# Optimization experiments

Measured on AMD Instinct MI355X. Metric: run time of the kernel, lower is better.

Reference implementation:

```python
import jax, jax.numpy as jnp
import numpy as np
import math

B, S, H = 2, 2048, 2048
NH, NKV, HD = 16, 8, 128          # heads, kv heads, head_dim
GROUPS = NH // NKV                 # 2
FF = 5632
EPS = 1e-6
SCALE = 0.02


def setup_inputs() -> dict:
    key = jax.random.key(0)
    ks = jax.random.split(key, 12)
    def w(k, shape):
        return jax.random.normal(k, shape, dtype=jnp.float32) * SCALE
    # additive causal mask: 0 on/below diagonal, -inf above
    causal = jnp.where(jnp.tril(jnp.ones((S, S), dtype=bool)), 0.0, -jnp.inf)
    attention_mask = causal[None, None].astype(jnp.float32)  # [1,1,S,S]
    return {
        "hidden_states": jax.random.normal(ks[0], (B, S, H), dtype=jnp.float32),
        "attention_mask": attention_mask,
        "q_w": w(ks[1], (NH * HD, H)),      # nn.Linear convention [out, in]
        "k_w": w(ks[2], (NKV * HD, H)),
        "v_w": w(ks[3], (NKV * HD, H)),
        "o_w": w(ks[4], (H, NH * HD)),
        "gate_w": w(ks[5], (FF, H)),
        "up_w": w(ks[6], (FF, H)),
        "down_w": w(ks[7], (H, FF)),
        "ln1_w": jnp.ones((H,), dtype=jnp.float32),
        "ln2_w": jnp.ones((H,), dtype=jnp.float32),
    }


def rmsnorm(x, w):
    var = jnp.mean(jnp.square(x), axis=-1, keepdims=True)
    return x * jax.lax.rsqrt(var + EPS) * w


def attention(x, mask, q_w, k_w, v_w, o_w):
    b, s, _ = x.shape
    q = (x @ q_w.T).reshape(b, s, NH, HD).transpose(0, 2, 1, 3)    # [b,nh,s,hd]
    k = (x @ k_w.T).reshape(b, s, NKV, HD).transpose(0, 2, 1, 3)   # [b,nkv,s,hd]
    v = (x @ v_w.T).reshape(b, s, NKV, HD).transpose(0, 2, 1, 3)
    # GQA: repeat_interleave kv heads to match query heads
    k = jnp.repeat(k, GROUPS, axis=1)
    v = jnp.repeat(v, GROUPS, axis=1)
    scores = jnp.einsum("bhqd,bhkd->bhqk", q, k) / math.sqrt(HD) + mask
    probs = jax.nn.softmax(scores.astype(jnp.float32), axis=-1).astype(q.dtype)
    out = jnp.einsum("bhqk,bhkd->bhqd", probs, v)
    out = out.transpose(0, 2, 1, 3).reshape(b, s, NH * HD)
    return out @ o_w.T


def mlp(x, gate_w, up_w, down_w):
    return (jax.nn.silu(x @ gate_w.T) * (x @ up_w.T)) @ down_w.T


def reference(hidden_states, attention_mask, q_w, k_w, v_w, o_w,
              gate_w, up_w, down_w, ln1_w, ln2_w):
    # pre-norm transformer layer with residuals
    h = hidden_states + attention(rmsnorm(hidden_states, ln1_w), attention_mask,
                                  q_w, k_w, v_w, o_w)
    out = h + mlp(rmsnorm(h, ln2_w), gate_w, up_w, down_w)
    return out
```

## Files before the change

kernel.cpp:

```cpp
#include <hip/hip_runtime.h>
#include <stdint.h>

typedef __bf16 bf16_t;
typedef __bf16 bf16x8 __attribute__((ext_vector_type(8)));
typedef __bf16 bf16x4 __attribute__((ext_vector_type(4)));
typedef float  f32x4  __attribute__((ext_vector_type(4)));

#define MFMA16(a, b, c) __builtin_amdgcn_mfma_f32_16x16x32_bf16((a), (b), (c), 0, 0, 0)

__device__ __forceinline__ void load_lds16(const bf16_t* g, bf16_t* l)
{
    __builtin_amdgcn_global_load_lds(
        (const __attribute__((address_space(1))) uint32_t*)(uintptr_t)g,
        (__attribute__((address_space(3))) uint32_t*)(uint32_t)(uintptr_t)l,
        16, 0, 0);
}

__global__ __launch_bounds__(256)
void wconv(const float* __restrict__ X, bf16_t* __restrict__ Y, int n)
{
    int i = (blockIdx.x * 256 + threadIdx.x) * 8;
    if (i >= n) return;
    f32x4 a = *(const f32x4*)(X + i);
    f32x4 b = *(const f32x4*)(X + i + 4);
    bf16x8 y;
#pragma unroll
    for (int e = 0; e < 4; ++e) { y[e] = (bf16_t)a[e]; y[e + 4] = (bf16_t)b[e]; }
    *(bf16x8*)(Y + i) = y;
}

__global__ __launch_bounds__(256)
void rmsnorm_f32(const float* __restrict__ X, const float* __restrict__ Wt,
                 bf16_t* __restrict__ Y)
{
    __shared__ float red[4];
    const int tid = threadIdx.x;
    const size_t row = blockIdx.x;
    const float* x = X + row * 2048;

    f32x4 x0 = *(const f32x4*)(x + tid * 8);
    f32x4 x1 = *(const f32x4*)(x + tid * 8 + 4);
    float ss = 0.f;
#pragma unroll
    for (int e = 0; e < 4; ++e) ss += x0[e] * x0[e] + x1[e] * x1[e];
#pragma unroll
    for (int off = 32; off; off >>= 1) ss += __shfl_xor(ss, off, 64);
    if ((tid & 63) == 0) red[tid >> 6] = ss;
    __syncthreads();
    float tot = red[0] + red[1] + red[2] + red[3];
    float scale = rsqrtf(tot * (1.f / 2048.f) + 1e-6f);

    f32x4 w0 = *(const f32x4*)(Wt + tid * 8);
    f32x4 w1 = *(const f32x4*)(Wt + tid * 8 + 4);
    bf16x8 yv;
#pragma unroll
    for (int e = 0; e < 4; ++e) {
        yv[e]     = (bf16_t)(x0[e] * scale * w0[e]);
        yv[e + 4] = (bf16_t)(x1[e] * scale * w1[e]);
    }
    *(bf16x8*)(Y + row * 2048 + tid * 8) = yv;
}

__global__ __launch_bounds__(256)
void rmsnorm_bf16(const bf16_t* __restrict__ X, const float* __restrict__ Wt,
                  bf16_t* __restrict__ Y)
{
    __shared__ float red[4];
    const int tid = threadIdx.x;
    const size_t row = blockIdx.x;

    bf16x8 xv = *(const bf16x8*)(X + row * 2048 + tid * 8);
    float xf[8];
    float ss = 0.f;
#pragma unroll
    for (int e = 0; e < 8; ++e) { xf[e] = (float)xv[e]; ss += xf[e] * xf[e]; }
#pragma unroll
    for (int off = 32; off; off >>= 1) ss += __shfl_xor(ss, off, 64);
    if ((tid & 63) == 0) red[tid >> 6] = ss;
    __syncthreads();
    float tot = red[0] + red[1] + red[2] + red[3];
    float scale = rsqrtf(tot * (1.f / 2048.f) + 1e-6f);

    f32x4 w0 = *(const f32x4*)(Wt + tid * 8);
    f32x4 w1 = *(const f32x4*)(Wt + tid * 8 + 4);
    bf16x8 yv;
#pragma unroll
    for (int e = 0; e < 4; ++e) {
        yv[e]     = (bf16_t)(xf[e] * scale * w0[e]);
        yv[e + 4] = (bf16_t)(xf[e + 4] * scale * w1[e]);
    }
    *(bf16x8*)(Y + row * 2048 + tid * 8) = yv;
}

__global__ __launch_bounds__(256, 2)
void gemm_bb(const bf16_t* __restrict__ A, const bf16_t* __restrict__ W,
             const float* __restrict__ Rf, const bf16_t* __restrict__ Rb,
             bf16_t* __restrict__ Cb, float* __restrict__ Cf,
             int M, int N, int K, int mode)
{
    __shared__ bf16_t As[128 * 64];
    __shared__ bf16_t Ws[128 * 64];

    const int tid  = threadIdx.x;
    const int lane = tid & 63, wave = tid >> 6;
    const int quad = lane >> 4, l16 = lane & 15;
    const int m0 = blockIdx.y * 128, n0 = blockIdx.x * 128;
    const int wm = (wave >> 1) * 64, wn = (wave & 1) * 64;

    const bf16_t* Ab = A + (size_t)(m0 + (tid >> 3)) * K + ((tid & 7) << 3);
    const bf16_t* Wb = W + (size_t)(n0 + (tid >> 3)) * K + ((tid & 7) << 3);

    f32x4 acc[4][4] = {};

    for (int k0 = 0; k0 < K; k0 += 64) {
        __syncthreads();
#pragma unroll
        for (int i = 0; i < 4; ++i) {
            load_lds16(Ab + (size_t)(i * 32) * K + k0, As + (i * 256 + tid) * 8);
            load_lds16(Wb + (size_t)(i * 32) * K + k0, Ws + (i * 256 + tid) * 8);
        }
        __syncthreads();

#pragma unroll
        for (int ks = 0; ks < 64; ks += 32) {
            bf16x8 af[4], bfr[4];
#pragma unroll
            for (int i = 0; i < 4; ++i)
                af[i] = *(const bf16x8*)(As + (wm + i * 16 + l16) * 64 + ks + quad * 8);
#pragma unroll
            for (int j = 0; j < 4; ++j)
                bfr[j] = *(const bf16x8*)(Ws + (wn + j * 16 + l16) * 64 + ks + quad * 8);
#pragma unroll
            for (int i = 0; i < 4; ++i)
#pragma unroll
                for (int j = 0; j < 4; ++j)
                    acc[i][j] = MFMA16(af[i], bfr[j], acc[i][j]);
        }
    }

#pragma unroll
    for (int i = 0; i < 4; ++i)
#pragma unroll
        for (int j = 0; j < 4; ++j)
#pragma unroll
            for (int r = 0; r < 4; ++r) {
                size_t row = (size_t)(m0 + wm + i * 16 + quad * 4 + r);
                size_t col = (size_t)(n0 + wn + j * 16 + l16);
                float v = acc[i][j][r];
                if (mode == 1) v += Rf[row * (size_t)N + col];
                if (mode == 2)
                    Cf[row * (size_t)N + col] = v + (float)Rb[row * (size_t)N + col];
                else
                    Cb[row * (size_t)N + col] = (bf16_t)v;
            }
}

__device__ __forceinline__ void stage_gu(const bf16_t* __restrict__ Ab,
                                         const bf16_t* __restrict__ Gb,
                                         const bf16_t* __restrict__ Ub,
                                         bf16_t* As, bf16_t* Gs, bf16_t* Us,
                                         int tid, int K, int k0)
{
#pragma unroll
    for (int l = 0; l < 4; ++l) {
        int u = l * 512 + tid;
        int row = u >> 3;
        int col = (((u & 7) ^ (row & 7)) << 3);
        load_lds16(Ab + (size_t)row * K + k0 + col, As + u * 8);
    }
#pragma unroll
    for (int l = 0; l < 2; ++l) {
        int u = l * 512 + tid;
        int row = u >> 3;
        int col = (((u & 7) ^ (row & 7)) << 3);
        load_lds16(Gb + (size_t)row * K + k0 + col, Gs + u * 8);
        load_lds16(Ub + (size_t)row * K + k0 + col, Us + u * 8);
    }
}

__global__ __launch_bounds__(512, 2)
void gateup8(const bf16_t* __restrict__ A, const bf16_t* __restrict__ G,
             const bf16_t* __restrict__ U, bf16_t* __restrict__ C,
             int M, int N, int K)
{
    __shared__ bf16_t As[2][256 * 64];
    __shared__ bf16_t Gs[2][128 * 64];
    __shared__ bf16_t Us[2][128 * 64];

    const int tid  = threadIdx.x;
    const int lane = tid & 63;
    const int wave = tid >> 6;
    const int quad = lane >> 4, l16 = lane & 15;
    const int wr = wave >> 2, wc = wave & 3;

    const int lid = (int)blockIdx.x;
    const int nwg = (M >> 8) * (N >> 7);
    const int cpx = nwg >> 3;
    const int swz = (lid & 7) * cpx + (lid >> 3);
    const int bxn = swz >> 4;
    const int bym = swz & 15;
    const int m0 = bym * 256, n0 = bxn * 128;

    const bf16_t* Ab = A + (size_t)m0 * K;
    const bf16_t* Gb = G + (size_t)n0 * K;
    const bf16_t* Ub = U + (size_t)n0 * K;

    const int xsw  = (l16 & 7) << 3;
    const int aoff = (wr * 128 + l16) * 64;
    const int boff = (wc * 32 + l16) * 64;

    f32x4 accg[8][2] = {};
    f32x4 accu[8][2] = {};

    stage_gu(Ab, Gb, Ub, As[0], Gs[0], Us[0], tid, K, 0);

    const int NT = K >> 6;
    for (int t = 0; t < NT; ++t) {
        const int b = t & 1;
        if (t + 1 < NT) {
            stage_gu(Ab, Gb, Ub, As[1 - b], Gs[1 - b], Us[1 - b],
                     tid, K, (t + 1) << 6);
            asm volatile("s_waitcnt vmcnt(8)" ::: "memory");
        } else {
            asm volatile("s_waitcnt vmcnt(0)" ::: "memory");
        }
        __builtin_amdgcn_s_barrier();

        const bf16_t* Asb = As[b];
        const bf16_t* Gsb = Gs[b];
        const bf16_t* Usb = Us[b];

#pragma unroll
        for (int ks = 0; ks < 64; ks += 32) {
            const int kxo = (ks + quad * 8) ^ xsw;
            bf16x8 af[8], bb[2];
#pragma unroll
            for (int i = 0; i < 8; ++i)
                af[i] = *(const bf16x8*)(Asb + aoff + i * 1024 + kxo);
#pragma unroll
            for (int j = 0; j < 2; ++j)
                bb[j] = *(const bf16x8*)(Gsb + boff + j * 1024 + kxo);
            __builtin_amdgcn_s_barrier();
            __builtin_amdgcn_s_setprio(1);
#pragma unroll
            for (int i = 0; i < 8; ++i)
#pragma unroll
                for (int j = 0; j < 2; ++j)
                    accg[i][j] = MFMA16(af[i], bb[j], accg[i][j]);
            __builtin_amdgcn_s_setprio(0);
            __builtin_amdgcn_s_barrier();
#pragma unroll
            for (int j = 0; j < 2; ++j)
                bb[j] = *(const bf16x8*)(Usb + boff + j * 1024 + kxo);
            __builtin_amdgcn_s_barrier();
            __builtin_amdgcn_s_setprio(1);
#pragma unroll
            for (int i = 0; i < 8; ++i)
#pragma unroll
                for (int j = 0; j < 2; ++j)
                    accu[i][j] = MFMA16(af[i], bb[j], accu[i][j]);
            __builtin_amdgcn_s_setprio(0);
            __builtin_amdgcn_s_barrier();
        }
    }

#pragma unroll
    for (int i = 0; i < 8; ++i)
#pragma unroll
        for (int j = 0; j < 2; ++j)
#pragma unroll
            for (int r = 0; r < 4; ++r) {
                size_t row = (size_t)(m0 + wr * 128 + i * 16 + quad * 4 + r);
                size_t col = (size_t)(n0 + wc * 32 + j * 16 + l16);
                float g = accg[i][j][r];
                float u = accu[i][j][r];
                float sig = 1.f / (1.f + __expf(fminf(-g, 80.f)));
                C[row * (size_t)N + col] = (bf16_t)(g * sig * u);
            }
}

__global__ __launch_bounds__(256, 2)
void gemm_bt(const bf16_t* __restrict__ A, const float* __restrict__ W,
             const float* __restrict__ Rf, const bf16_t* __restrict__ Rb,
             bf16_t* __restrict__ Cb, float* __restrict__ Cf,
             int M, int N, int K, int mode)
{
    __shared__ bf16_t As[128 * 64];
    __shared__ bf16_t Ws[128 * 64];

    const int tid  = threadIdx.x;
    const int lane = tid & 63, wave = tid >> 6;
    const int quad = lane >> 4, l16 = lane & 15;
    const int m0 = blockIdx.y * 128, n0 = blockIdx.x * 128;
    const int wm = (wave >> 1) * 64, wn = (wave & 1) * 64;

    f32x4 acc[4][4] = {};

    for (int k0 = 0; k0 < K; k0 += 64) {
        bf16x8 ra[4];
        bf16x4 rw[8];
#pragma unroll
        for (int i = 0; i < 4; ++i) {
            int u = i * 256 + tid;
            int r = u >> 3, c = (u & 7) << 3;
            ra[i] = *(const bf16x8*)(A + (size_t)(m0 + r) * K + k0 + c);
        }
#pragma unroll
        for (int i = 0; i < 8; ++i) {
            int u = i * 256 + tid;
            int r = u >> 4, c = (u & 15) << 2;
            f32x4 w4 = *(const f32x4*)(W + (size_t)(n0 + r) * K + k0 + c);
#pragma unroll
            for (int e = 0; e < 4; ++e) rw[i][e] = (bf16_t)w4[e];
        }
        __syncthreads();
#pragma unroll
        for (int i = 0; i < 4; ++i)
            *(bf16x8*)(As + (i * 256 + tid) * 8) = ra[i];
#pragma unroll
        for (int i = 0; i < 8; ++i)
            *(bf16x4*)(Ws + (i * 256 + tid) * 4) = rw[i];
        __syncthreads();

#pragma unroll
        for (int ks = 0; ks < 64; ks += 32) {
            bf16x8 af[4], bfr[4];
#pragma unroll
            for (int i = 0; i < 4; ++i)
                af[i] = *(const bf16x8*)(As + (wm + i * 16 + l16) * 64 + ks + quad * 8);
#pragma unroll
            for (int j = 0; j < 4; ++j)
                bfr[j] = *(const bf16x8*)(Ws + (wn + j * 16 + l16) * 64 + ks + quad * 8);
#pragma unroll
            for (int i = 0; i < 4; ++i)
#pragma unroll
                for (int j = 0; j < 4; ++j)
                    acc[i][j] = MFMA16(af[i], bfr[j], acc[i][j]);
        }
    }

#pragma unroll
    for (int i = 0; i < 4; ++i)
#pragma unroll
        for (int j = 0; j < 4; ++j)
#pragma unroll
            for (int r = 0; r < 4; ++r) {
                size_t row = (size_t)(m0 + wm + i * 16 + quad * 4 + r);
                size_t col = (size_t)(n0 + wn + j * 16 + l16);
                float v = acc[i][j][r];
                if (mode == 1) v += Rf[row * (size_t)N + col];
                if (mode == 2)
                    Cf[row * (size_t)N + col] = v + (float)Rb[row * (size_t)N + col];
                else
                    Cb[row * (size_t)N + col] = (bf16_t)v;
            }
}

__global__ __launch_bounds__(256, 2)
void gemm_gateup(const bf16_t* __restrict__ A, const float* __restrict__ G,
                 const float* __restrict__ U, bf16_t* __restrict__ C,
                 int M, int N, int K)
{
    __shared__ bf16_t As[128 * 64];
    __shared__ bf16_t Gs[128 * 64];
    __shared__ bf16_t Us[128 * 64];

    const int tid  = threadIdx.x;
    const int lane = tid & 63, wave = tid >> 6;
    const int quad = lane >> 4, l16 = lane & 15;
    const int m0 = blockIdx.y * 128, n0 = blockIdx.x * 128;
    const int wm = (wave >> 1) * 64, wn = (wave & 1) * 64;

    f32x4 accg[4][4] = {};
    f32x4 accu[4][4] = {};

    for (int k0 = 0; k0 < K; k0 += 64) {
        bf16x8 ra[4];
        bf16x4 rg[8], ru[8];
#pragma unroll
        for (int i = 0; i < 4; ++i) {
            int u = i * 256 + tid;
            int r = u >> 3, c = (u & 7) << 3;
            ra[i] = *(const bf16x8*)(A + (size_t)(m0 + r) * K + k0 + c);
        }
#pragma unroll
        for (int i = 0; i < 8; ++i) {
            int u = i * 256 + tid;
            int r = u >> 4, c = (u & 15) << 2;
            f32x4 g4 = *(const f32x4*)(G + (size_t)(n0 + r) * K + k0 + c);
            f32x4 u4 = *(const f32x4*)(U + (size_t)(n0 + r) * K + k0 + c);
#pragma unroll
            for (int e = 0; e < 4; ++e) { rg[i][e] = (bf16_t)g4[e]; ru[i][e] = (bf16_t)u4[e]; }
        }
        __syncthreads();
#pragma unroll
        for (int i = 0; i < 4; ++i)
            *(bf16x8*)(As + (i * 256 + tid) * 8) = ra[i];
#pragma unroll
        for (int i = 0; i < 8; ++i) {
            *(bf16x4*)(Gs + (i * 256 + tid) * 4) = rg[i];
            *(bf16x4*)(Us + (i * 256 + tid) * 4) = ru[i];
        }
        __syncthreads();

#pragma unroll
        for (int ks = 0; ks < 64; ks += 32) {
            bf16x8 af[4], bg[4], bu[4];
#pragma unroll
            for (int i = 0; i < 4; ++i)
                af[i] = *(const bf16x8*)(As + (wm + i * 16 + l16) * 64 + ks + quad * 8);
#pragma unroll
            for (int j = 0; j < 4; ++j) {
                bg[j] = *(const bf16x8*)(Gs + (wn + j * 16 + l16) * 64 + ks + quad * 8);
                bu[j] = *(const bf16x8*)(Us + (wn + j * 16 + l16) * 64 + ks + quad * 8);
            }
#pragma unroll
            for (int i = 0; i < 4; ++i)
#pragma unroll
                for (int j = 0; j < 4; ++j) {
                    accg[i][j] = MFMA16(af[i], bg[j], accg[i][j]);
                    accu[i][j] = MFMA16(af[i], bu[j], accu[i][j]);
                }
        }
    }

#pragma unroll
    for (int i = 0; i < 4; ++i)
#pragma unroll
        for (int j = 0; j < 4; ++j)
#pragma unroll
            for (int r = 0; r < 4; ++r) {
                size_t row = (size_t)(m0 + wm + i * 16 + quad * 4 + r);
                size_t col = (size_t)(n0 + wn + j * 16 + l16);
                float g = accg[i][j][r];
                float u = accu[i][j][r];
                float sig = 1.f / (1.f + __expf(fminf(-g, 80.f)));
                C[row * (size_t)N + col] = (bf16_t)(g * sig * u);
            }
}

__global__ __launch_bounds__(256, 2)
void attn_fwd(const bf16_t* __restrict__ Q, const bf16_t* __restrict__ Kg,
              const bf16_t* __restrict__ Vg, bf16_t* __restrict__ O)
{
    __shared__ bf16_t Ks[64 * 128];
    __shared__ bf16_t Vt[128 * 64];
    __shared__ bf16_t Pl[4][16 * 72];

    const int tid  = threadIdx.x;
    const int lane = tid & 63, wave = tid >> 6;
    const int quad = lane >> 4, l16 = lane & 15;
    const int bh = blockIdx.y, b = bh >> 4, h = bh & 15;

    const bf16_t* Qh = Q  + (size_t)b * 2048 * 2048 + (size_t)h * 128;
    const bf16_t* Kh = Kg + (size_t)b * 2048 * 1024 + (size_t)(h >> 1) * 128;
    const bf16_t* Vh = Vg + (size_t)b * 2048 * 1024 + (size_t)(h >> 1) * 128;

    const float scale = 0.08838834764831845f;

#pragma unroll 1
    for (int pass = 0; pass < 2; ++pass) {
        const int qt = pass ? (31 - (int)blockIdx.x) : (int)blockIdx.x;
        const int q0 = qt * 64;

        bf16x8 aq[4];
#pragma unroll
        for (int ks = 0; ks < 4; ++ks)
            aq[ks] = *(const bf16x8*)(Qh + (size_t)(q0 + wave * 16 + l16) * 2048 + ks * 32 + quad * 8);

        float m_r[4] = { -30000.f, -30000.f, -30000.f, -30000.f };
        float l_r[4] = { 0.f, 0.f, 0.f, 0.f };
        f32x4 acc_o[8] = {};

        const int ntiles = qt + 1;

        for (int t = 0; t < ntiles; ++t) {
            const int kv0 = t * 64;
            __syncthreads();
#pragma unroll
            for (int i = 0; i < 4; ++i) {
                int u = i * 256 + tid;
                int rk = u >> 4, c = (u & 15) << 3;
                *(bf16x8*)(Ks + u * 8) =
                    *(const bf16x8*)(Kh + (size_t)(kv0 + rk) * 1024 + c);
            }
#pragma unroll
            for (int it = 0; it < 4; ++it) {
                int v = it * 256 + tid;
                int d = v & 127, kb = v >> 7;
                bf16x8 vt8;
#pragma unroll
                for (int j = 0; j < 8; ++j)
                    vt8[j] = Vh[(size_t)(kv0 + kb * 8 + j) * 1024 + d];
                *(bf16x8*)(Vt + d * 64 + ((kb ^ (d & 7)) << 3)) = vt8;
            }
            __syncthreads();

            f32x4 accs[4] = {};
#pragma unroll
            for (int ks = 0; ks < 4; ++ks)
#pragma unroll
                for (int j = 0; j < 4; ++j) {
                    bf16x8 bk = *(const bf16x8*)(Ks + (j * 16 + l16) * 128 + ks * 32 + quad * 8);
                    accs[j] = MFMA16(aq[ks], bk, accs[j]);
                }

#pragma unroll
            for (int r = 0; r < 4; ++r) {
                const int qrow = q0 + wave * 16 + quad * 4 + r;
                float s[4];
                float mx = -30000.f;
#pragma unroll
                for (int j = 0; j < 4; ++j) {
                    s[j] = accs[j][r] * scale;
                    if (kv0 + j * 16 + l16 > qrow) s[j] = -30000.f;
                    mx = fmaxf(mx, s[j]);
                }
                mx = fmaxf(mx, __shfl_xor(mx, 1, 64));
                mx = fmaxf(mx, __shfl_xor(mx, 2, 64));
                mx = fmaxf(mx, __shfl_xor(mx, 4, 64));
                mx = fmaxf(mx, __shfl_xor(mx, 8, 64));
                float mnew  = fmaxf(m_r[r], mx);
                float alpha = __expf(fmaxf(m_r[r] - mnew, -80.f));
                float rs = 0.f;
#pragma unroll
                for (int j = 0; j < 4; ++j) {
                    float p = __expf(fmaxf(s[j] - mnew, -80.f));
                    rs += p;
                    Pl[wave][(quad * 4 + r) * 72 + j * 16 + l16] = (bf16_t)p;
                }
                rs += __shfl_xor(rs, 1, 64);
                rs += __shfl_xor(rs, 2, 64);
                rs += __shfl_xor(rs, 4, 64);
                rs += __shfl_xor(rs, 8, 64);
                l_r[r] = l_r[r] * alpha + rs;
                m_r[r] = mnew;
#pragma unroll
                for (int nt = 0; nt < 8; ++nt) acc_o[nt][r] *= alpha;
            }

            __syncthreads();

#pragma unroll
            for (int ks2 = 0; ks2 < 2; ++ks2) {
                bf16x8 ap = *(const bf16x8*)(&Pl[wave][l16 * 72 + ks2 * 32 + quad * 8]);
                const int kb_r = ks2 * 4 + quad;
#pragma unroll
                for (int nt = 0; nt < 8; ++nt) {
                    const int d = nt * 16 + l16;
                    bf16x8 bv = *(const bf16x8*)(Vt + d * 64 + ((kb_r ^ (d & 7)) << 3));
                    acc_o[nt] = MFMA16(ap, bv, acc_o[nt]);
                }
            }
        }

#pragma unroll
        for (int r = 0; r < 4; ++r) {
            float inv = 1.f / fmaxf(l_r[r], 1e-30f);
            size_t orow = (size_t)b * 2048 + q0 + wave * 16 + quad * 4 + r;
#pragma unroll
            for (int nt = 0; nt < 8; ++nt)
                O[orow * 2048 + h * 128 + nt * 16 + l16] = (bf16_t)(acc_o[nt][r] * inv);
        }
    }
}

extern "C" void kernel_launch(void* const* d_in, const int* in_sizes, int n_in,
                              void* d_out, int out_size, void* d_ws, size_t ws_size,
                              hipStream_t stream)
{
    const float* x   = (const float*)d_in[0];
    const float* qw  = (const float*)d_in[2];
    const float* kw  = (const float*)d_in[3];
    const float* vw  = (const float*)d_in[4];
    const float* ow  = (const float*)d_in[5];
    const float* gw  = (const float*)d_in[6];
    const float* uw  = (const float*)d_in[7];
    const float* dw  = (const float*)d_in[8];
    const float* ln1 = (const float*)d_in[9];
    const float* ln2 = (const float*)d_in[10];
    float*  out = (float*)d_out;
    bf16_t* ws  = (bf16_t*)d_ws;

    dim3 blk(256);
    const size_t NEED = 87031808ull * 2;

    if (ws_size >= NEED) {
        bf16_t* wq = ws;
        bf16_t* wk = ws + 4194304;
        bf16_t* wv = ws + 6291456;
        bf16_t* wo = ws + 8388608;
        bf16_t* wg = ws + 12582912;
        bf16_t* wu = ws + 24117248;
        bf16_t* wd = ws + 35651584;
        bf16_t* h1 = ws + 47185920;
        bf16_t* qb = ws + 55574528;
        bf16_t* kb = ws + 63963136;
        bf16_t* vb = ws + 68157440;
        bf16_t* ab = (bf16_t*)d_out;
        bf16_t* hb = qb;
        bf16_t* gb = kb;

        wconv<<<2048, blk, 0, stream>>>(qw, wq, 4194304);
        wconv<<<1024, blk, 0, stream>>>(kw, wk, 2097152);
        wconv<<<1024, blk, 0, stream>>>(vw, wv, 2097152);
        wconv<<<2048, blk, 0, stream>>>(ow, wo, 4194304);
        wconv<<<5632, blk, 0, stream>>>(gw, wg, 11534336);
        wconv<<<5632, blk, 0, stream>>>(uw, wu, 11534336);
        wconv<<<5632, blk, 0, stream>>>(dw, wd, 11534336);

        rmsnorm_f32<<<4096, blk, 0, stream>>>(x, ln1, h1);
        gemm_bb<<<dim3(16, 32), blk, 0, stream>>>(h1, wq, nullptr, nullptr, qb, nullptr, 4096, 2048, 2048, 0);
        gemm_bb<<<dim3( 8, 32), blk, 0, stream>>>(h1, wk, nullptr, nullptr, kb, nullptr, 4096, 1024, 2048, 0);
        gemm_bb<<<dim3( 8, 32), blk, 0, stream>>>(h1, wv, nullptr, nullptr, vb, nullptr, 4096, 1024, 2048, 0);
        attn_fwd<<<dim3(16, 32), blk, 0, stream>>>(qb, kb, vb, ab);
        gemm_bb<<<dim3(16, 32), blk, 0, stream>>>(ab, wo, x, nullptr, hb, nullptr, 4096, 2048, 2048, 1);
        rmsnorm_bf16<<<4096, blk, 0, stream>>>(hb, ln2, h1);
        gateup8<<<704, dim3(512), 0, stream>>>(h1, wg, wu, gb, 4096, 5632, 2048);
        gemm_bb<<<dim3(16, 32), blk, 0, stream>>>(gb, wd, nullptr, hb, nullptr, out, 4096, 2048, 5632, 2);
    } else {
        const size_t ME = 1ull << 20;
        bf16_t* h1 = ws;
        bf16_t* qb = ws + 8  * ME;
        bf16_t* kb = ws + 16 * ME;
        bf16_t* vb = ws + 20 * ME;
        bf16_t* ab = (bf16_t*)d_out;
        bf16_t* hb = ws + 8  * ME;
        bf16_t* gb = ws + 16 * ME;

        rmsnorm_f32<<<4096, blk, 0, stream>>>(x, ln1, h1);
        gemm_bt<<<dim3(16, 32), blk, 0, stream>>>(h1, qw, nullptr, nullptr, qb, nullptr, 4096, 2048, 2048, 0);
        gemm_bt<<<dim3( 8, 32), blk, 0, stream>>>(h1, kw, nullptr, nullptr, kb, nullptr, 4096, 1024, 2048, 0);
        gemm_bt<<<dim3( 8, 32), blk, 0, stream>>>(h1, vw, nullptr, nullptr, vb, nullptr, 4096, 1024, 2048, 0);
        attn_fwd<<<dim3(16, 32), blk, 0, stream>>>(qb, kb, vb, ab);
        gemm_bt<<<dim3(16, 32), blk, 0, stream>>>(ab, ow, x, nullptr, hb, nullptr, 4096, 2048, 2048, 1);
        rmsnorm_bf16<<<4096, blk, 0, stream>>>(hb, ln2, h1);
        gemm_gateup<<<dim3(44, 32), blk, 0, stream>>>(h1, gw, uw, gb, 4096, 5632, 2048);
        gemm_bt<<<dim3(16, 32), blk, 0, stream>>>(gb, dw, nullptr, hb, nullptr, out, 4096, 2048, 5632, 2);
    }
}
```

Before: 964.3 us.

## Add 256x128 8-wave GEMM and interleave prefetch with MFMA in gate-up

Adds gemm8, a 512-thread kernel with 256x128 tiles, a swizzled block order and double buffering, and uses it for the Q, O and down projections in place of gemm_bb. The next K-tile's global-to-LDS loads are split into pieces and issued between MFMA phases, so each wait only needs the current tile. The gate-up kernel is restructured the same way: gate and up fragments are loaded together, the A rows are processed in two halves, and the G/U/A prefetches are interleaved with the compute. This aims to hide load latency and shrink the exposed wait at each tile boundary. The cost is more barriers per tile and a larger 512-thread block, which may lower occupancy.

```diff
diff --git a/kernel.cpp b/kernel.cpp
--- a/kernel.cpp
+++ b/kernel.cpp
@@ -14,6 +14,19 @@
         (const __attribute__((address_space(1))) uint32_t*)(uintptr_t)g,
         (__attribute__((address_space(3))) uint32_t*)(uint32_t)(uintptr_t)l,
         16, 0, 0);
+}
+
+__device__ __forceinline__ void lds_stage2(const bf16_t* __restrict__ Gsrc,
+                                           bf16_t* Ldst, int u0,
+                                           int tid, int K, int k0)
+{
+#pragma unroll
+    for (int l = 0; l < 2; ++l) {
+        int u = u0 + l * 512 + tid;
+        int row = u >> 3;
+        int col = (((u & 7) ^ (row & 7)) << 3);
+        load_lds16(Gsrc + (size_t)row * K + k0 + col, Ldst + u * 8);
+    }
 }
 
 __global__ __launch_bounds__(256)
@@ -155,27 +168,99 @@
             }
 }
 
-__device__ __forceinline__ void stage_gu(const bf16_t* __restrict__ Ab,
-                                         const bf16_t* __restrict__ Gb,
-                                         const bf16_t* __restrict__ Ub,
-                                         bf16_t* As, bf16_t* Gs, bf16_t* Us,
-                                         int tid, int K, int k0)
-{
-#pragma unroll
-    for (int l = 0; l < 4; ++l) {
-        int u = l * 512 + tid;
-        int row = u >> 3;
-        int col = (((u & 7) ^ (row & 7)) << 3);
-        load_lds16(Ab + (size_t)row * K + k0 + col, As + u * 8);
-    }
-#pragma unroll
-    for (int l = 0; l < 2; ++l) {
-        int u = l * 512 + tid;
-        int row = u >> 3;
-        int col = (((u & 7) ^ (row & 7)) << 3);
-        load_lds16(Gb + (size_t)row * K + k0 + col, Gs + u * 8);
-        load_lds16(Ub + (size_t)row * K + k0 + col, Us + u * 8);
-    }
+__global__ __launch_bounds__(512, 2)
+void gemm8(const bf16_t* __restrict__ A, const bf16_t* __restrict__ W,
+           const float* __restrict__ Rf, const bf16_t* __restrict__ Rb,
+           bf16_t* __restrict__ Cb, float* __restrict__ Cf,
+           int M, int N, int K, int mode)
+{
+    __shared__ bf16_t As[2][256 * 64];
+    __shared__ bf16_t Ws[2][128 * 64];
+
+    const int tid  = threadIdx.x;
+    const int lane = tid & 63, wave = tid >> 6;
+    const int quad = lane >> 4, l16 = lane & 15;
+    const int wr = wave >> 1, wc = wave & 1;
+
+    const int lid = (int)blockIdx.x;
+    const int swz = (lid & 7) * 32 + (lid >> 3);
+    const int bym = swz >> 4;
+    const int bxn = swz & 15;
+    const int m0 = bym * 256, n0 = bxn * 128;
+
+    const bf16_t* Ab = A + (size_t)m0 * K;
+    const bf16_t* Wb = W + (size_t)n0 * K;
+
+    const int xsw  = (l16 & 7) << 3;
+    const int aoff = (wr * 64 + l16) * 64;
+    const int boff = (wc * 64 + l16) * 64;
+
+    f32x4 acc[4][4] = {};
+
+    lds_stage2(Ab, As[0], 0,    tid, K, 0);
+    lds_stage2(Ab, As[0], 1024, tid, K, 0);
+    lds_stage2(Wb, Ws[0], 0,    tid, K, 0);
+
+    const int NT = K >> 6;
+    for (int t = 0; t < NT; ++t) {
+        const int b  = t & 1;
+        const int kn = (t + 1) << 6;
+        const bool pf = (t + 1 < NT);
+        bf16_t* An = As[1 - b];
+        bf16_t* Wn = Ws[1 - b];
+
+        if (pf) {
+            lds_stage2(Ab, An, 0, tid, K, kn);
+            asm volatile("s_waitcnt vmcnt(2)" ::: "memory");
+        } else {
+            asm volatile("s_waitcnt vmcnt(0)" ::: "memory");
+        }
+        __builtin_amdgcn_s_barrier();
+
+        const bf16_t* Asb = As[b];
+        const bf16_t* Wsb = Ws[b];
+
+#pragma unroll
+        for (int ks = 0; ks < 2; ++ks) {
+            const int kxo = (ks * 32 + quad * 8) ^ xsw;
+            bf16x8 af[4], bf_[4];
+#pragma unroll
+            for (int i = 0; i < 4; ++i)
+                af[i] = *(const bf16x8*)(Asb + aoff + i * 1024 + kxo);
+#pragma unroll
+            for (int j = 0; j < 4; ++j)
+                bf_[j] = *(const bf16x8*)(Wsb + boff + j * 1024 + kxo);
+            if (pf) {
+                if (ks == 0) lds_stage2(Ab, An, 1024, tid, K, kn);
+                else         lds_stage2(Wb, Wn, 0,    tid, K, kn);
+            }
+            __builtin_amdgcn_s_barrier();
+            __builtin_amdgcn_s_setprio(1);
+#pragma unroll
+            for (int i = 0; i < 4; ++i)
+#pragma unroll
+                for (int j = 0; j < 4; ++j)
+                    acc[i][j] = MFMA16(af[i], bf_[j], acc[i][j]);
+            __builtin_amdgcn_s_setprio(0);
+            __builtin_amdgcn_s_barrier();
+        }
+    }
+
+#pragma unroll
+    for (int i = 0; i < 4; ++i)
+#pragma unroll
+        for (int j = 0; j < 4; ++j)
+#pragma unroll
+            for (int r = 0; r < 4; ++r) {
+                size_t row = (size_t)(m0 + wr * 64 + i * 16 + quad * 4 + r);
+                size_t col = (size_t)(n0 + wc * 64 + j * 16 + l16);
+                float v = acc[i][j][r];
+                if (mode == 1) v += Rf[row * (size_t)N + col];
+                if (mode == 2)
+                    Cf[row * (size_t)N + col] = v + (float)Rb[row * (size_t)N + col];
+                else
+                    Cb[row * (size_t)N + col] = (bf16_t)v;
+            }
 }
 
 __global__ __launch_bounds__(512, 2)
@@ -212,15 +297,23 @@
     f32x4 accg[8][2] = {};
     f32x4 accu[8][2] = {};
 
-    stage_gu(Ab, Gb, Ub, As[0], Gs[0], Us[0], tid, K, 0);
+    lds_stage2(Ab, As[0], 0,    tid, K, 0);
+    lds_stage2(Ab, As[0], 1024, tid, K, 0);
+    lds_stage2(Gb, Gs[0], 0,    tid, K, 0);
+    lds_stage2(Ub, Us[0], 0,    tid, K, 0);
 
     const int NT = K >> 6;
     for (int t = 0; t < NT; ++t) {
-        const int b = t & 1;
-        if (t + 1 < NT) {
-            stage_gu(Ab, Gb, Ub, As[1 - b], Gs[1 - b], Us[1 - b],
-                     tid, K, (t + 1) << 6);
-            asm volatile("s_waitcnt vmcnt(8)" ::: "memory");
+        const int b  = t & 1;
+        const int kn = (t + 1) << 6;
+        const bool pf = (t + 1 < NT);
+        bf16_t* An = As[1 - b];
+        bf16_t* Gn = Gs[1 - b];
+        bf16_t* Un = Us[1 - b];
+
+        if (pf) {
+            lds_stage2(Ab, An, 0, tid, K, kn);
+            asm volatile("s_waitcnt vmcnt(2)" ::: "memory");
         } else {
             asm volatile("s_waitcnt vmcnt(0)" ::: "memory");
         }
@@ -230,38 +323,92 @@
         const bf16_t* Gsb = Gs[b];
         const bf16_t* Usb = Us[b];
 
-#pragma unroll
-        for (int ks = 0; ks < 64; ks += 32) {
-            const int kxo = (ks + quad * 8) ^ xsw;
-            bf16x8 af[8], bb[2];
-#pragma unroll
-            for (int i = 0; i < 8; ++i)
+        bf16x8 af[4], bg[2], bu[2];
+
+        {
+            const int kxo = (quad * 8) ^ xsw;
+#pragma unroll
+            for (int i = 0; i < 4; ++i)
                 af[i] = *(const bf16x8*)(Asb + aoff + i * 1024 + kxo);
 #pragma unroll
-            for (int j = 0; j < 2; ++j)
-                bb[j] = *(const bf16x8*)(Gsb + boff + j * 1024 + kxo);
-            __builtin_amdgcn_s_barrier();
-            __builtin_amdgcn_s_setprio(1);
-#pragma unroll
-            for (int i = 0; i < 8; ++i)
-#pragma unroll
-                for (int j = 0; j < 2; ++j)
-                    accg[i][j] = MFMA16(af[i], bb[j], accg[i][j]);
-            __builtin_amdgcn_s_setprio(0);
-            __builtin_amdgcn_s_barrier();
-#pragma unroll
-            for (int j = 0; j < 2; ++j)
-                bb[j] = *(const bf16x8*)(Usb + boff + j * 1024 + kxo);
-            __builtin_amdgcn_s_barrier();
-            __builtin_amdgcn_s_setprio(1);
-#pragma unroll
-            for (int i = 0; i < 8; ++i)
-#pragma unroll
-                for (int j = 0; j < 2; ++j)
-                    accu[i][j] = MFMA16(af[i], bb[j], accu[i][j]);
-            __builtin_amdgcn_s_setprio(0);
-            __builtin_amdgcn_s_barrier();
-        }
+            for (int j = 0; j < 2; ++j) {
+                bg[j] = *(const bf16x8*)(Gsb + boff + j * 1024 + kxo);
+                bu[j] = *(const bf16x8*)(Usb + boff + j * 1024 + kxo);
+            }
+        }
+        if (pf) lds_stage2(Ab, An, 1024, tid, K, kn);
+        __builtin_amdgcn_s_barrier();
+        __builtin_amdgcn_s_setprio(1);
+#pragma unroll
+        for (int i = 0; i < 4; ++i)
+#pragma unroll
+            for (int j = 0; j < 2; ++j) {
+                accg[i][j] = MFMA16(af[i], bg[j], accg[i][j]);
+                accu[i][j] = MFMA16(af[i], bu[j], accu[i][j]);
+            }
+        __builtin_amdgcn_s_setprio(0);
+        __builtin_amdgcn_s_barrier();
+
+        {
+            const int kxo = (quad * 8) ^ xsw;
+#pragma unroll
+            for (int i = 0; i < 4; ++i)
+                af[i] = *(const bf16x8*)(Asb + aoff + (i + 4) * 1024 + kxo);
+        }
+        if (pf) lds_stage2(Gb, Gn, 0, tid, K, kn);
+        __builtin_amdgcn_s_barrier();
+        __builtin_amdgcn_s_setprio(1);
+#pragma unroll
+        for (int i = 0; i < 4; ++i)
+#pragma unroll
+            for (int j = 0; j < 2; ++j) {
+                accg[i + 4][j] = MFMA16(af[i], bg[j], accg[i + 4][j]);
+                accu[i + 4][j] = MFMA16(af[i], bu[j], accu[i + 4][j]);
+            }
+        __builtin_amdgcn_s_setprio(0);
+        __builtin_amdgcn_s_barrier();
+
+        {
+            const int kxo = (32 + quad * 8) ^ xsw;
+#pragma unroll
+            for (int i = 0; i < 4; ++i)
+                af[i] = *(const bf16x8*)(Asb + aoff + i * 1024 + kxo);
+#pragma unroll
+            for (int j = 0; j < 2; ++j) {
+                bg[j] = *(const bf16x8*)(Gsb + boff + j * 1024 + kxo);
+                bu[j] = *(const bf16x8*)(Usb + boff + j * 1024 + kxo);
+            }
+        }
+        if (pf) lds_stage2(Ub, Un, 0, tid, K, kn);
+        __builtin_amdgcn_s_barrier();
+        __builtin_amdgcn_s_setprio(1);
+#pragma unroll
+        for (int i = 0; i < 4; ++i)
+#pragma unroll
+            for (int j = 0; j < 2; ++j) {
+                accg[i][j] = MFMA16(af[i], bg[j], accg[i][j]);
+                accu[i][j] = MFMA16(af[i], bu[j], accu[i][j]);
+            }
+        __builtin_amdgcn_s_setprio(0);
+        __builtin_amdgcn_s_barrier();
+
+        {
+            const int kxo = (32 + quad * 8) ^ xsw;
+#pragma unroll
+            for (int i = 0; i < 4; ++i)
+                af[i] = *(const bf16x8*)(Asb + aoff + (i + 4) * 1024 + kxo);
+        }
+        __builtin_amdgcn_s_barrier();
+        __builtin_amdgcn_s_setprio(1);
+#pragma unroll
+        for (int i = 0; i < 4; ++i)
+#pragma unroll
+            for (int j = 0; j < 2; ++j) {
+                accg[i + 4][j] = MFMA16(af[i], bg[j], accg[i + 4][j]);
+                accu[i + 4][j] = MFMA16(af[i], bu[j], accu[i + 4][j]);
+            }
+        __builtin_amdgcn_s_setprio(0);
+        __builtin_amdgcn_s_barrier();
     }
 
 #pragma unroll
@@ -610,14 +757,14 @@
         wconv<<<5632, blk, 0, stream>>>(dw, wd, 11534336);
 
         rmsnorm_f32<<<4096, blk, 0, stream>>>(x, ln1, h1);
-        gemm_bb<<<dim3(16, 32), blk, 0, stream>>>(h1, wq, nullptr, nullptr, qb, nullptr, 4096, 2048, 2048, 0);
+        gemm8<<<256, dim3(512), 0, stream>>>(h1, wq, nullptr, nullptr, qb, nullptr, 4096, 2048, 2048, 0);
         gemm_bb<<<dim3( 8, 32), blk, 0, stream>>>(h1, wk, nullptr, nullptr, kb, nullptr, 4096, 1024, 2048, 0);
         gemm_bb<<<dim3( 8, 32), blk, 0, stream>>>(h1, wv, nullptr, nullptr, vb, nullptr, 4096, 1024, 2048, 0);
         attn_fwd<<<dim3(16, 32), blk, 0, stream>>>(qb, kb, vb, ab);
-        gemm_bb<<<dim3(16, 32), blk, 0, stream>>>(ab, wo, x, nullptr, hb, nullptr, 4096, 2048, 2048, 1);
+        gemm8<<<256, dim3(512), 0, stream>>>(ab, wo, x, nullptr, hb, nullptr, 4096, 2048, 2048, 1);
         rmsnorm_bf16<<<4096, blk, 0, stream>>>(hb, ln2, h1);
         gateup8<<<704, dim3(512), 0, stream>>>(h1, wg, wu, gb, 4096, 5632, 2048);
-        gemm_bb<<<dim3(16, 32), blk, 0, stream>>>(gb, wd, nullptr, hb, nullptr, out, 4096, 2048, 5632, 2);
+        gemm8<<<256, dim3(512), 0, stream>>>(gb, wd, nullptr, hb, nullptr, out, 4096, 2048, 5632, 2);
     } else {
         const size_t ME = 1ull << 20;
         bf16_t* h1 = ws;
```

Result: faster. 887.2 us (-8.0%).
